# Performance work log

Hardware: AMD Instinct MI355X
Metric: run time of the kernel (lower is better)

## Reference

```python
import jax, jax.numpy as jnp
import numpy as np

B, T, D = 2048, 200, 256

def setup_inputs() -> dict:
    key = jax.random.key(0)
    k1, k2, k3, k4, k5 = jax.random.split(key, 5)
    query = jax.random.normal(k1, (B, 1, D), dtype=jnp.float32)
    user_behavior = jax.random.normal(k2, (B, T, D), dtype=jnp.float32)
    mask = jax.random.bernoulli(k3, 0.5, (B, T))
    # nn.Linear weights: linear1 (2D -> D), linear2 (D -> 1), no bias
    W1 = jax.random.normal(k4, (D, 2 * D), dtype=jnp.float32) * (1.0 / np.sqrt(2 * D))
    W2 = jax.random.normal(k5, (1, D), dtype=jnp.float32) * (1.0 / np.sqrt(D))
    return {"query": query, "user_behavior": user_behavior, "mask": mask, "W1": W1, "W2": W2}

def reference(query, user_behavior, mask, W1, W2):
    T_ = user_behavior.shape[1]
    queries = jnp.broadcast_to(query, (query.shape[0], T_, query.shape[2]))  # [B,T,D]
    attn_in = jnp.concatenate([queries, user_behavior], axis=-1)  # [B,T,2D]
    h = jnp.tanh(jnp.einsum('btk,dk->btd', attn_in, W1))          # [B,T,D]
    score = jnp.einsum('btd,od->bot', h, W2)                       # [B,1,T] (transpose(1,2) of [B,T,1])
    # masked_fill with 0 BEFORE softmax, as in the original module
    score = jnp.where(mask[:, None, :], jnp.zeros((), score.dtype), score)
    attn = jax.nn.softmax(score, axis=-1)                          # [B,1,T]
    out = jnp.matmul(attn, user_behavior)                          # [B,1,D]
    return jnp.squeeze(out)                                        # [B,D]
```

## Files before the change

kernel.cpp:

```cpp
#include <hip/hip_runtime.h>
#include <hip/hip_bf16.h>

typedef __bf16 bf16_t;
typedef __bf16 bf16x8 __attribute__((ext_vector_type(8)));
typedef float  f32x4  __attribute__((ext_vector_type(4)));

#define T_LEN 200
#define D_DIM 256
#define NTILE 13

__device__ __forceinline__ float fast_tanh(float x) {
    float e = __expf(2.0f * x);
    return 1.0f - 2.0f / (e + 1.0f);
}

__global__ __launch_bounds__(256) void qpart_kernel(
    const float* __restrict__ Q, const float* __restrict__ W1,
    float* __restrict__ Out)
{
    __shared__ float qs[8][256];
    const int tid = threadIdx.x;
    const int b0  = blockIdx.x * 8;
    for (int idx = tid; idx < 8 * 256; idx += 256)
        qs[idx >> 8][idx & 255] = Q[(size_t)(b0 + (idx >> 8)) * 256 + (idx & 255)];
    __syncthreads();
    float acc[8];
    #pragma unroll
    for (int i = 0; i < 8; ++i) acc[i] = 0.f;
    const f32x4* Wv = (const f32x4*)(W1 + (size_t)tid * 512);
    #pragma unroll 4
    for (int k4 = 0; k4 < 64; ++k4) {
        f32x4 w = Wv[k4];
        #pragma unroll
        for (int bb = 0; bb < 8; ++bb) {
            f32x4 qv = *(const f32x4*)&qs[bb][k4 * 4];
            acc[bb] += qv[0]*w[0] + qv[1]*w[1] + qv[2]*w[2] + qv[3]*w[3];
        }
    }
    #pragma unroll
    for (int bb = 0; bb < 8; ++bb)
        Out[(size_t)(b0 + bb) * 256 + tid] = acc[bb];
}

__global__ __launch_bounds__(512, 4) void attn_main_kernel(
    const float* __restrict__ U,
    const int*   __restrict__ Mask,
    const float* __restrict__ W1,
    const float* __restrict__ W2,
    float* __restrict__ Out)
{
    __shared__ bf16_t ubt[3][16 * 256];
    __shared__ float score_lds[208];
    __shared__ float p_lds[208];
    __shared__ float out_lds[4][256];
    __shared__ float l_lds;

    const int tid  = threadIdx.x;
    const int lane = tid & 63;
    const int wv   = tid >> 6;
    const int lr   = lane & 15;
    const int lg   = lane >> 4;
    const int b    = blockIdx.x;

    bf16x8 bq[2][8];
    float  w2v[2];
    #pragma unroll
    for (int n = 0; n < 2; ++n) {
        const int d = wv * 32 + n * 16 + lr;
        const float* wrow = W1 + (size_t)d * 512 + 256;
        #pragma unroll
        for (int kk = 0; kk < 8; ++kk) {
            const float* s = wrow + kk * 32 + lg * 8;
            f32x4 lo = *(const f32x4*)s;
            f32x4 hi = *(const f32x4*)(s + 4);
            bf16x8 v;
            v[0]=(bf16_t)lo[0]; v[1]=(bf16_t)lo[1]; v[2]=(bf16_t)lo[2]; v[3]=(bf16_t)lo[3];
            v[4]=(bf16_t)hi[0]; v[5]=(bf16_t)hi[1]; v[6]=(bf16_t)hi[2]; v[7]=(bf16_t)hi[3];
            bq[n][kk] = v;
        }
        w2v[n] = W2[d];
    }

    const float* Ub = U + (size_t)b * (T_LEN * D_DIM);

    float qp[2];
    #pragma unroll
    for (int n = 0; n < 2; ++n)
        qp[n] = Out[(size_t)b * 256 + wv * 32 + n * 16 + lr];

    if (tid < 208) score_lds[tid] = 0.f;
    if (tid == 0)  l_lds = 0.f;

    const int srow = tid >> 5;
    const int scol = (tid & 31) * 8;
    const unsigned swoff = (unsigned)srow * 512
                         + (((unsigned)scol * 2) ^ (((unsigned)srow & 7) << 4));

    {
        const float* src = Ub + (size_t)srow * 256 + scol;
        f32x4 g0 = *(const f32x4*)src;
        f32x4 g1 = *(const f32x4*)(src + 4);
        bf16x8 v;
        v[0]=(bf16_t)g0[0]; v[1]=(bf16_t)g0[1]; v[2]=(bf16_t)g0[2]; v[3]=(bf16_t)g0[3];
        v[4]=(bf16_t)g1[0]; v[5]=(bf16_t)g1[1]; v[6]=(bf16_t)g1[2]; v[7]=(bf16_t)g1[3];
        *(bf16x8*)((char*)&ubt[0][0] + swoff) = v;
    }
    __syncthreads();

    for (int it = 0; it < NTILE; ++it) {
        char* const bcur = (char*)&ubt[it % 3][0];
        char* const bnxt = (char*)&ubt[(it + 1) % 3][0];

        f32x4 g0 = {0.f,0.f,0.f,0.f}, g1 = {0.f,0.f,0.f,0.f};
        bool stage_w = false;
        if (it + 1 < NTILE) {
            const int t = (it + 1) * 16 + srow;
            if (t < T_LEN) {
                const float* src = Ub + (size_t)t * 256 + scol;
                g0 = *(const f32x4*)src;
                g1 = *(const f32x4*)(src + 4);
                stage_w = true;
            }
        }

        f32x4 acc0 = {0.f,0.f,0.f,0.f}, acc1 = {0.f,0.f,0.f,0.f};
        #pragma unroll
        for (int kk = 0; kk < 8; ++kk) {
            const unsigned kb   = (unsigned)(kk * 64 + lg * 16);
            const unsigned aoff = (unsigned)lr * 512
                                + (kb ^ (((unsigned)lr & 7) << 4));
            bf16x8 a = *(const bf16x8*)(bcur + aoff);
            acc0 = __builtin_amdgcn_mfma_f32_16x16x32_bf16(a, bq[0][kk], acc0, 0, 0, 0);
            acc1 = __builtin_amdgcn_mfma_f32_16x16x32_bf16(a, bq[1][kk], acc1, 0, 0, 0);
        }

        if (stage_w) {
            bf16x8 v;
            v[0]=(bf16_t)g0[0]; v[1]=(bf16_t)g0[1]; v[2]=(bf16_t)g0[2]; v[3]=(bf16_t)g0[3];
            v[4]=(bf16_t)g1[0]; v[5]=(bf16_t)g1[1]; v[6]=(bf16_t)g1[2]; v[7]=(bf16_t)g1[3];
            *(bf16x8*)(bnxt + swoff) = v;
        }

        float sp[4];
        #pragma unroll
        for (int r = 0; r < 4; ++r) {
            float h0 = fast_tanh(acc0[r] + qp[0]);
            float h1 = fast_tanh(acc1[r] + qp[1]);
            sp[r] = h0 * w2v[0] + h1 * w2v[1];
        }
        #pragma unroll
        for (int r = 0; r < 4; ++r) {
            sp[r] += __shfl_xor(sp[r], 1);
            sp[r] += __shfl_xor(sp[r], 2);
            sp[r] += __shfl_xor(sp[r], 4);
            sp[r] += __shfl_xor(sp[r], 8);
        }
        if (lr == 0) {
            #pragma unroll
            for (int r = 0; r < 4; ++r)
                atomicAdd(&score_lds[it * 16 + lg * 4 + r], sp[r]);
        }

        __syncthreads();
    }

    {
        float p = 0.f;
        if (tid < T_LEN)
            p = Mask[(size_t)b * T_LEN + tid] ? 1.0f : __expf(score_lds[tid]);
        if (tid < 208) p_lds[tid] = p;
        float ps = p;
        ps += __shfl_xor(ps, 1);
        ps += __shfl_xor(ps, 2);
        ps += __shfl_xor(ps, 4);
        ps += __shfl_xor(ps, 8);
        ps += __shfl_xor(ps, 16);
        ps += __shfl_xor(ps, 32);
        if (lane == 0 && ps != 0.f) atomicAdd(&l_lds, ps);
    }
    __syncthreads();

    {
        const int dp = tid & 127;
        const int jg = tid >> 7;
        float o0 = 0.f, o1 = 0.f;
        const float* Up = Ub + (size_t)(jg * 50) * 256 + dp * 2;
        #pragma unroll 5
        for (int i = 0; i < 50; ++i) {
            const float p = p_lds[jg * 50 + i];
            const float2 u = *(const float2*)(Up + (size_t)i * 256);
            o0 += p * u.x;
            o1 += p * u.y;
        }
        out_lds[jg][dp * 2]     = o0;
        out_lds[jg][dp * 2 + 1] = o1;
    }
    __syncthreads();

    if (tid < 256) {
        const float o = out_lds[0][tid] + out_lds[1][tid]
                      + out_lds[2][tid] + out_lds[3][tid];
        Out[(size_t)b * 256 + tid] = o / l_lds;
    }
}

extern "C" void kernel_launch(void* const* d_in, const int* in_sizes, int n_in,
                              void* d_out, int out_size, void* d_ws, size_t ws_size,
                              hipStream_t stream)
{
    const float* Q  = (const float*)d_in[0];
    const float* U  = (const float*)d_in[1];
    const int*   Mk = (const int*)d_in[2];
    const float* W1 = (const float*)d_in[3];
    const float* W2 = (const float*)d_in[4];
    float* Out = (float*)d_out;
    const int B = in_sizes[0] / D_DIM;

    qpart_kernel<<<dim3(B / 8), dim3(256), 0, stream>>>(Q, W1, Out);
    attn_main_kernel<<<dim3(B), dim3(512), 0, stream>>>(U, Mk, W1, W2, Out);
}
```

Measured before the change: 225.1 us.

## Split sequence across two blocks, keep bf16 tile resident in LDS for reuse

The main kernel now loads a block's whole slice of user_behavior into LDS as bf16 once and reuses it for both the score GEMM and the weighted sum. This removes the second global read of U in fp32 and the per-tile barriers. Each batch row is split into two blocks over time (7 and 6 tiles) that write partial numerators and softmax denominators to workspace, and a combine kernel adds them. W1 is pre-converted to bf16 by a separate kernel. The costs are two extra launches, extra workspace traffic, and less precision in the weighted sum because it now reads bf16 values instead of fp32.

```diff
diff --git a/kernel.cpp b/kernel.cpp
--- a/kernel.cpp
+++ b/kernel.cpp
@@ -2,12 +2,12 @@
 #include <hip/hip_bf16.h>
 
 typedef __bf16 bf16_t;
-typedef __bf16 bf16x8 __attribute__((ext_vector_type(8)));
-typedef float  f32x4  __attribute__((ext_vector_type(4)));
+typedef __bf16 bf16x4_t __attribute__((ext_vector_type(4)));
+typedef __bf16 bf16x8  __attribute__((ext_vector_type(8)));
+typedef float  f32x4   __attribute__((ext_vector_type(4)));
 
 #define T_LEN 200
 #define D_DIM 256
-#define NTILE 13
 
 __device__ __forceinline__ float fast_tanh(float x) {
     float e = __expf(2.0f * x);
@@ -42,16 +42,29 @@
         Out[(size_t)(b0 + bb) * 256 + tid] = acc[bb];
 }
 
-__global__ __launch_bounds__(512, 4) void attn_main_kernel(
+__global__ __launch_bounds__(256) void convw_kernel(
+    const float* __restrict__ W1, bf16_t* __restrict__ bfW)
+{
+    const int d = blockIdx.x;
+    const int k = threadIdx.x;
+    bfW[(size_t)d * 256 + k] = (bf16_t)W1[(size_t)d * 512 + 256 + k];
+}
+
+template<bool SPLIT>
+__global__ __launch_bounds__(512, SPLIT ? 4 : 2) void attn_fused_kernel(
     const float* __restrict__ U,
     const int*   __restrict__ Mask,
     const float* __restrict__ W1,
     const float* __restrict__ W2,
-    float* __restrict__ Out)
-{
-    __shared__ bf16_t ubt[3][16 * 256];
-    __shared__ float score_lds[208];
-    __shared__ float p_lds[208];
+    const bf16_t* __restrict__ bfW,
+    float* Out,
+    float* __restrict__ WsNum,
+    float* __restrict__ WsL)
+{
+    constexpr int MAXT = SPLIT ? 7 : 13;
+    __shared__ bf16_t tiles[MAXT * 16 * 256];
+    __shared__ float score_lds[MAXT * 16];
+    __shared__ float p_lds[MAXT * 16];
     __shared__ float out_lds[4][256];
     __shared__ float l_lds;
 
@@ -60,87 +73,81 @@
     const int wv   = tid >> 6;
     const int lr   = lane & 15;
     const int lg   = lane >> 4;
-    const int b    = blockIdx.x;
+
+    int b, t0, ntile;
+    if (SPLIT) {
+        b = blockIdx.x >> 1;
+        const int h = blockIdx.x & 1;
+        t0 = h ? 112 : 0;
+        ntile = h ? 6 : 7;
+    } else {
+        b = blockIdx.x; t0 = 0; ntile = 13;
+    }
+    const int rows = ntile * 16;
+    char* const tbase = (char*)tiles;
+
+    if (tid < rows) score_lds[tid] = 0.f;
+    if (tid == 0)   l_lds = 0.f;
+
+    {
+        const float* Ub = U + (size_t)b * (T_LEN * D_DIM);
+        #pragma unroll 2
+        for (int r = wv; r < rows; r += 8) {
+            const int t = t0 + r;
+            bf16x4_t v;
+            v[0] = (bf16_t)0.f; v[1] = (bf16_t)0.f;
+            v[2] = (bf16_t)0.f; v[3] = (bf16_t)0.f;
+            if (t < T_LEN) {
+                f32x4 g = *(const f32x4*)(Ub + (size_t)t * 256 + lane * 4);
+                v[0] = (bf16_t)g[0]; v[1] = (bf16_t)g[1];
+                v[2] = (bf16_t)g[2]; v[3] = (bf16_t)g[3];
+            }
+            *(bf16x4_t*)(tbase + r * 512 + ((lane * 8) ^ ((r & 7) << 4))) = v;
+        }
+    }
 
     bf16x8 bq[2][8];
     float  w2v[2];
     #pragma unroll
     for (int n = 0; n < 2; ++n) {
         const int d = wv * 32 + n * 16 + lr;
-        const float* wrow = W1 + (size_t)d * 512 + 256;
-        #pragma unroll
-        for (int kk = 0; kk < 8; ++kk) {
-            const float* s = wrow + kk * 32 + lg * 8;
-            f32x4 lo = *(const f32x4*)s;
-            f32x4 hi = *(const f32x4*)(s + 4);
-            bf16x8 v;
-            v[0]=(bf16_t)lo[0]; v[1]=(bf16_t)lo[1]; v[2]=(bf16_t)lo[2]; v[3]=(bf16_t)lo[3];
-            v[4]=(bf16_t)hi[0]; v[5]=(bf16_t)hi[1]; v[6]=(bf16_t)hi[2]; v[7]=(bf16_t)hi[3];
-            bq[n][kk] = v;
+        if (SPLIT) {
+            #pragma unroll
+            for (int kk = 0; kk < 8; ++kk)
+                bq[n][kk] = *(const bf16x8*)(bfW + (size_t)d * 256 + kk * 32 + lg * 8);
+        } else {
+            const float* wrow = W1 + (size_t)d * 512 + 256;
+            #pragma unroll
+            for (int kk = 0; kk < 8; ++kk) {
+                const float* s = wrow + kk * 32 + lg * 8;
+                f32x4 lo = *(const f32x4*)s;
+                f32x4 hi = *(const f32x4*)(s + 4);
+                bf16x8 v;
+                v[0]=(bf16_t)lo[0]; v[1]=(bf16_t)lo[1]; v[2]=(bf16_t)lo[2]; v[3]=(bf16_t)lo[3];
+                v[4]=(bf16_t)hi[0]; v[5]=(bf16_t)hi[1]; v[6]=(bf16_t)hi[2]; v[7]=(bf16_t)hi[3];
+                bq[n][kk] = v;
+            }
         }
         w2v[n] = W2[d];
     }
-
-    const float* Ub = U + (size_t)b * (T_LEN * D_DIM);
-
     float qp[2];
     #pragma unroll
     for (int n = 0; n < 2; ++n)
         qp[n] = Out[(size_t)b * 256 + wv * 32 + n * 16 + lr];
 
-    if (tid < 208) score_lds[tid] = 0.f;
-    if (tid == 0)  l_lds = 0.f;
-
-    const int srow = tid >> 5;
-    const int scol = (tid & 31) * 8;
-    const unsigned swoff = (unsigned)srow * 512
-                         + (((unsigned)scol * 2) ^ (((unsigned)srow & 7) << 4));
-
-    {
-        const float* src = Ub + (size_t)srow * 256 + scol;
-        f32x4 g0 = *(const f32x4*)src;
-        f32x4 g1 = *(const f32x4*)(src + 4);
-        bf16x8 v;
-        v[0]=(bf16_t)g0[0]; v[1]=(bf16_t)g0[1]; v[2]=(bf16_t)g0[2]; v[3]=(bf16_t)g0[3];
-        v[4]=(bf16_t)g1[0]; v[5]=(bf16_t)g1[1]; v[6]=(bf16_t)g1[2]; v[7]=(bf16_t)g1[3];
-        *(bf16x8*)((char*)&ubt[0][0] + swoff) = v;
-    }
-    __syncthreads();
-
-    for (int it = 0; it < NTILE; ++it) {
-        char* const bcur = (char*)&ubt[it % 3][0];
-        char* const bnxt = (char*)&ubt[(it + 1) % 3][0];
-
-        f32x4 g0 = {0.f,0.f,0.f,0.f}, g1 = {0.f,0.f,0.f,0.f};
-        bool stage_w = false;
-        if (it + 1 < NTILE) {
-            const int t = (it + 1) * 16 + srow;
-            if (t < T_LEN) {
-                const float* src = Ub + (size_t)t * 256 + scol;
-                g0 = *(const f32x4*)src;
-                g1 = *(const f32x4*)(src + 4);
-                stage_w = true;
-            }
-        }
-
+    __syncthreads();
+
+    for (int mt = 0; mt < ntile; ++mt) {
         f32x4 acc0 = {0.f,0.f,0.f,0.f}, acc1 = {0.f,0.f,0.f,0.f};
+        const int rbase = mt * 16 + lr;
         #pragma unroll
         for (int kk = 0; kk < 8; ++kk) {
-            const unsigned kb   = (unsigned)(kk * 64 + lg * 16);
-            const unsigned aoff = (unsigned)lr * 512
-                                + (kb ^ (((unsigned)lr & 7) << 4));
-            bf16x8 a = *(const bf16x8*)(bcur + aoff);
+            const unsigned aoff = (unsigned)rbase * 512
+                + (((unsigned)(kk * 64 + lg * 16)) ^ (((unsigned)lr & 7) << 4));
+            bf16x8 a = *(const bf16x8*)(tbase + aoff);
             acc0 = __builtin_amdgcn_mfma_f32_16x16x32_bf16(a, bq[0][kk], acc0, 0, 0, 0);
             acc1 = __builtin_amdgcn_mfma_f32_16x16x32_bf16(a, bq[1][kk], acc1, 0, 0, 0);
         }
-
-        if (stage_w) {
-            bf16x8 v;
-            v[0]=(bf16_t)g0[0]; v[1]=(bf16_t)g0[1]; v[2]=(bf16_t)g0[2]; v[3]=(bf16_t)g0[3];
-            v[4]=(bf16_t)g1[0]; v[5]=(bf16_t)g1[1]; v[6]=(bf16_t)g1[2]; v[7]=(bf16_t)g1[3];
-            *(bf16x8*)(bnxt + swoff) = v;
-        }
-
         float sp[4];
         #pragma unroll
         for (int r = 0; r < 4; ++r) {
@@ -158,17 +165,17 @@
         if (lr == 0) {
             #pragma unroll
             for (int r = 0; r < 4; ++r)
-                atomicAdd(&score_lds[it * 16 + lg * 4 + r], sp[r]);
-        }
-
-        __syncthreads();
-    }
+                atomicAdd(&score_lds[mt * 16 + lg * 4 + r], sp[r]);
+        }
+    }
+    __syncthreads();
 
     {
         float p = 0.f;
-        if (tid < T_LEN)
-            p = Mask[(size_t)b * T_LEN + tid] ? 1.0f : __expf(score_lds[tid]);
-        if (tid < 208) p_lds[tid] = p;
+        const int t = t0 + tid;
+        if (tid < rows && t < T_LEN)
+            p = Mask[(size_t)b * T_LEN + t] ? 1.0f : __expf(score_lds[tid]);
+        if (tid < rows) p_lds[tid] = p;
         float ps = p;
         ps += __shfl_xor(ps, 1);
         ps += __shfl_xor(ps, 2);
@@ -183,14 +190,15 @@
     {
         const int dp = tid & 127;
         const int jg = tid >> 7;
+        const int qr = rows >> 2;
         float o0 = 0.f, o1 = 0.f;
-        const float* Up = Ub + (size_t)(jg * 50) * 256 + dp * 2;
-        #pragma unroll 5
-        for (int i = 0; i < 50; ++i) {
-            const float p = p_lds[jg * 50 + i];
-            const float2 u = *(const float2*)(Up + (size_t)i * 256);
-            o0 += p * u.x;
-            o1 += p * u.y;
+        for (int i = 0; i < qr; ++i) {
+            const int j = jg * qr + i;
+            const float p = p_lds[j];
+            const unsigned w = *(const unsigned*)(tbase + j * 512
+                             + (((unsigned)(dp * 4)) ^ (((unsigned)j & 7) << 4)));
+            o0 += p * __builtin_bit_cast(float, w << 16);
+            o1 += p * __builtin_bit_cast(float, w & 0xffff0000u);
         }
         out_lds[jg][dp * 2]     = o0;
         out_lds[jg][dp * 2 + 1] = o1;
@@ -198,10 +206,23 @@
     __syncthreads();
 
     if (tid < 256) {
-        const float o = out_lds[0][tid] + out_lds[1][tid]
-                      + out_lds[2][tid] + out_lds[3][tid];
-        Out[(size_t)b * 256 + tid] = o / l_lds;
-    }
+        const float num = out_lds[0][tid] + out_lds[1][tid]
+                        + out_lds[2][tid] + out_lds[3][tid];
+        if (SPLIT) WsNum[(size_t)blockIdx.x * 256 + tid] = num;
+        else       Out[(size_t)b * 256 + tid] = num / l_lds;
+    }
+    if (SPLIT && tid == 0) WsL[blockIdx.x] = l_lds;
+}
+
+__global__ __launch_bounds__(256) void combine_kernel(
+    const float* __restrict__ WsNum, const float* __restrict__ WsL,
+    float* __restrict__ Out)
+{
+    const int b = blockIdx.x, tid = threadIdx.x;
+    const float n = WsNum[(size_t)(2 * b) * 256 + tid]
+                  + WsNum[(size_t)(2 * b + 1) * 256 + tid];
+    const float l = WsL[2 * b] + WsL[2 * b + 1];
+    Out[(size_t)b * 256 + tid] = n / l;
 }
 
 extern "C" void kernel_launch(void* const* d_in, const int* in_sizes, int n_in,
@@ -217,5 +238,21 @@
     const int B = in_sizes[0] / D_DIM;
 
     qpart_kernel<<<dim3(B / 8), dim3(256), 0, stream>>>(Q, W1, Out);
-    attn_main_kernel<<<dim3(B), dim3(512), 0, stream>>>(U, Mk, W1, W2, Out);
-}
+
+    const size_t nblk = (size_t)B * 2;
+    const size_t need = nblk * 256 * 4
+                      + nblk * 4
+                      + 256 * 256 * 2;
+    if (ws_size >= need) {
+        float*  wsn = (float*)d_ws;
+        float*  wsl = wsn + nblk * 256;
+        bf16_t* bfw = (bf16_t*)(wsl + nblk);
+        convw_kernel<<<dim3(256), dim3(256), 0, stream>>>(W1, bfw);
+        attn_fused_kernel<true><<<dim3((unsigned)nblk), dim3(512), 0, stream>>>(
+            U, Mk, W1, W2, bfw, Out, wsn, wsl);
+        combine_kernel<<<dim3(B), dim3(256), 0, stream>>>(wsn, wsl, Out);
+    } else {
+        attn_fused_kernel<false><<<dim3(B), dim3(512), 0, stream>>>(
+            U, Mk, W1, W2, nullptr, Out, nullptr, nullptr);
+    }
+}
```

After: 223.3 us. About the same (-0.8%).
